# Performance work log

Measured on AMD Instinct MI355X. Metric: run time of the kernel, lower is better.

The kernel has to match this reference:

```python
import jax, jax.numpy as jnp
import numpy as np
import math

B, C, H, W = 16, 512, 32, 32
GROUPS = 32
EPS = 1e-5


def group_norm(x, w, b):
    # x: [B, C, H, W]; normalize within each of GROUPS channel groups over (C//G, H, W)
    Bx, Cx, Hx, Wx = x.shape
    xg = x.reshape(Bx, GROUPS, Cx // GROUPS, Hx, Wx)
    mean = xg.mean(axis=(2, 3, 4), keepdims=True)
    var = xg.var(axis=(2, 3, 4), keepdims=True)
    xg = (xg - mean) * jax.lax.rsqrt(var + EPS)
    xn = xg.reshape(Bx, Cx, Hx, Wx)
    return xn * w[None, :, None, None] + b[None, :, None, None]


def setup_inputs() -> dict:
    key = jax.random.key(0)
    ks = jax.random.split(key, 4)
    x = jax.random.normal(ks[0], (B, C, H, W), dtype=jnp.float32)
    gn_w = jnp.ones((C,), dtype=jnp.float32)
    gn_b = jnp.zeros((C,), dtype=jnp.float32)
    # Conv2d 1x1 weights as [out, in] matrices; PyTorch default init scale
    qkv_w = jax.random.normal(ks[1], (3 * C, C), dtype=jnp.float32) * (1.0 / math.sqrt(C))
    qkv_b = jnp.zeros((3 * C,), dtype=jnp.float32)
    out_w = jax.random.normal(ks[2], (C, C), dtype=jnp.float32) * (1.0 / math.sqrt(C))
    out_b = jnp.zeros((C,), dtype=jnp.float32)
    return {"x": x, "gn_w": gn_w, "gn_b": gn_b, "qkv_w": qkv_w,
            "qkv_b": qkv_b, "out_w": out_w, "out_b": out_b}


def reference(x, gn_w, gn_b, qkv_w, qkv_b, out_w, out_b):
    Bx, Cx, Hx, Wx = x.shape
    N = Hx * Wx
    h = group_norm(x, gn_w, gn_b)                       # [B, C, H, W]
    hf = h.reshape(Bx, Cx, N)                           # [B, C, N]
    # 1x1 conv == channel matmul
    qkv = jnp.einsum('oc,bcn->bon', qkv_w, hf) + qkv_b[None, :, None]  # [B, 3C, N]
    q, k, v = jnp.split(qkv, 3, axis=1)                 # each [B, C, N]
    q = q.transpose(0, 2, 1)                            # [B, N, C]
    v = v.transpose(0, 2, 1)                            # [B, N, C]
    scale = 1.0 / math.sqrt(Cx)
    attn = jnp.einsum('bnc,bcm->bnm', q, k) * scale     # [B, N, N]
    attn = jax.nn.softmax(attn, axis=-1)
    o = jnp.einsum('bnm,bmc->bnc', attn, v)             # [B, N, C]
    o = o.transpose(0, 2, 1)                            # [B, C, N]
    o = jnp.einsum('oc,bcn->bon', out_w, o) + out_b[None, :, None]
    return x + o.reshape(Bx, Cx, Hx, Wx)
```

## Files before the change

### kernel.cpp

```cpp
#include <hip/hip_runtime.h>

typedef unsigned short u16;
typedef short short8 __attribute__((ext_vector_type(8)));
typedef float floatx4 __attribute__((ext_vector_type(4)));
typedef u16 u16x4 __attribute__((ext_vector_type(4)));
typedef u16 u16x8 __attribute__((ext_vector_type(8)));

#define DEVI __device__ __forceinline__

DEVI u16 f2bf(float x) {
    union { float f; unsigned u; } c; c.f = x;
    unsigned u = c.u;
    u += 0x7fffu + ((u >> 16) & 1u);
    return (u16)(u >> 16);
}
DEVI float bf2f(u16 h) {
    union { unsigned u; float f; } c; c.u = ((unsigned)h) << 16;
    return c.f;
}

DEVI void gload_lds16(const void* g, void* l) {
    auto gp = (const __attribute__((address_space(1))) unsigned*)(unsigned long long)g;
    auto lp = (__attribute__((address_space(3))) unsigned*)(unsigned)(unsigned long long)l;
    __builtin_amdgcn_global_load_lds(gp, lp, 16, 0, 0);
}

__global__ __launch_bounds__(256) void gn_fused_kernel(const float* __restrict__ x,
                                                       const float* __restrict__ w,
                                                       const float* __restrict__ bb,
                                                       u16* __restrict__ h) {
    const int bg = blockIdx.x;
    const int b = bg >> 5, g = bg & 31;
    const float* xg = x + (long long)bg * 16384;
    const int n0 = threadIdx.x * 4;

    float4 xv[16];
    float s = 0.f, s2 = 0.f;
    #pragma unroll
    for (int cc = 0; cc < 16; cc++) {
        xv[cc] = *(const float4*)&xg[cc * 1024 + n0];
        s  += xv[cc].x + xv[cc].y + xv[cc].z + xv[cc].w;
        s2 += xv[cc].x*xv[cc].x + xv[cc].y*xv[cc].y + xv[cc].z*xv[cc].z + xv[cc].w*xv[cc].w;
    }
    #pragma unroll
    for (int m = 1; m < 64; m <<= 1) { s += __shfl_xor(s, m, 64); s2 += __shfl_xor(s2, m, 64); }
    __shared__ float rs[4], rq[4];
    if ((threadIdx.x & 63) == 0) { rs[threadIdx.x >> 6] = s; rq[threadIdx.x >> 6] = s2; }
    __syncthreads();
    float mean = (rs[0] + rs[1] + rs[2] + rs[3]) * (1.f / 16384.f);
    float var  = (rq[0] + rq[1] + rq[2] + rq[3]) * (1.f / 16384.f) - mean * mean;
    float rstd = rsqrtf(var + 1e-5f);

    u16x8 o[4][2];
    #pragma unroll
    for (int cc = 0; cc < 16; cc++) {
        int c = g * 16 + cc;
        float sc = w[c] * rstd;
        float sh = bb[c] - mean * sc;
        o[0][cc >> 3][cc & 7] = f2bf(xv[cc].x * sc + sh);
        o[1][cc >> 3][cc & 7] = f2bf(xv[cc].y * sc + sh);
        o[2][cc >> 3][cc & 7] = f2bf(xv[cc].z * sc + sh);
        o[3][cc >> 3][cc & 7] = f2bf(xv[cc].w * sc + sh);
    }
    u16* hb = h + ((long long)b * 1024 + n0) * 512 + g * 16;
    #pragma unroll
    for (int k = 0; k < 4; k++) {
        *(u16x8*)&hb[(long long)k * 512]     = o[k][0];
        *(u16x8*)&hb[(long long)k * 512 + 8] = o[k][1];
    }
}

__global__ __launch_bounds__(256) void wconv_kernel(const float* __restrict__ w1, u16* __restrict__ o1,
                                                    const float* __restrict__ w2, u16* __restrict__ o2) {
    int i = blockIdx.x * 256 + threadIdx.x;
    const float* src; u16* dst; int j;
    if (i < 196608) { src = w1; dst = o1; j = i; }
    else            { src = w2; dst = o2; j = i - 196608; }
    float4 v = *(const float4*)&src[j * 4];
    u16x4 p; p[0] = f2bf(v.x); p[1] = f2bf(v.y); p[2] = f2bf(v.z); p[3] = f2bf(v.w);
    *(u16x4*)&dst[j * 4] = p;
}

__global__ __launch_bounds__(256) void softmax_kernel(u16* __restrict__ P) {
    const int lid  = blockIdx.x;
    const int xcd  = lid & 7;
    const int slot = lid >> 3;
    const int j    = slot >> 8;
    const int w    = slot & 255;
    const int z    = xcd + 8 * j;
    const int wave = threadIdx.x >> 6, lane = threadIdx.x & 63;
    const long long row = (long long)z * 1024 + w * 4 + wave;
    u16* p = P + row * 1024 + lane * 16;
    u16x8 a = *(u16x8*)p;
    u16x8 b = *(u16x8*)(p + 8);
    float v[16];
    #pragma unroll
    for (int k = 0; k < 8; k++) { v[k] = bf2f(a[k]); v[8+k] = bf2f(b[k]); }
    float mx = v[0];
    #pragma unroll
    for (int k = 1; k < 16; k++) mx = fmaxf(mx, v[k]);
    #pragma unroll
    for (int m = 1; m < 64; m <<= 1) mx = fmaxf(mx, __shfl_xor(mx, m, 64));
    float s = 0.f;
    #pragma unroll
    for (int k = 0; k < 16; k++) { v[k] = __expf(v[k] - mx); s += v[k]; }
    #pragma unroll
    for (int m = 1; m < 64; m <<= 1) s += __shfl_xor(s, m, 64);
    float inv = 1.f / s;
    #pragma unroll
    for (int k = 0; k < 8; k++) { a[k] = f2bf(v[k]*inv); b[k] = f2bf(v[8+k]*inv); }
    *(u16x8*)p = a;
    *(u16x8*)(p + 8) = b;
}

template <int MODE, int NX, int NY>
__global__ __launch_bounds__(256, 3)
void gemm_bt_kernel(const u16* __restrict__ A, const u16* __restrict__ Bt,
                    void* __restrict__ C0,
                    const float* __restrict__ bias, const float* __restrict__ res,
                    float scale, int lda, int ldb, int ldc,
                    long long sA, long long sB, long long sC, long long sR, int K) {
    int bx, by, bz;
    if (NX > 0) {
        const int lid  = blockIdx.x;
        const int xcd  = lid & 7;
        const int slot = lid >> 3;
        const int per  = NX * NY;
        const int j    = slot / per;
        const int w    = slot - j * per;
        bz = xcd + 8 * j;
        bx = w % NX;
        by = w / NX;
    } else {
        bx = blockIdx.x; by = blockIdx.y; bz = blockIdx.z;
    }
    const int t    = threadIdx.x;
    const int lane = t & 63;
    const int wave = t >> 6;
    const int m0   = by * 128;
    const int n0   = bx * 128;
    A  += (long long)bz * sA;
    Bt += (long long)bz * sB;

    __shared__ __align__(16) u16 smem[16384];
    u16* As = smem;
    u16* Bs = smem + 8192;

    const int wm = wave >> 1, wn = wave & 1;
    const int quad = lane >> 4, lrow = lane & 15;

    floatx4 acc[4][4];
    #pragma unroll
    for (int i = 0; i < 4; i++)
        #pragma unroll
        for (int j = 0; j < 4; j++)
            #pragma unroll
            for (int r = 0; r < 4; r++) acc[i][j][r] = 0.f;

    const int rowA = t >> 2;
    const int kch  = (t & 3) * 8;
    const u16* Ag = A  + (long long)(m0 + rowA) * lda + kch;
    const u16* Bg = Bt + (long long)(n0 + rowA) * ldb + kch;
    u16* Al = &As[t * 8];
    u16* Bl = &Bs[t * 8];
    const long long a64 = (long long)64 * lda;
    const long long b64 = (long long)64 * ldb;

    for (int k0 = 0; k0 < K; k0 += 64) {
        gload_lds16(Ag + k0,            Al);
        gload_lds16(Ag + k0 + a64,      Al + 2048);
        gload_lds16(Ag + k0 + 32,       Al + 4096);
        gload_lds16(Ag + k0 + 32 + a64, Al + 6144);
        gload_lds16(Bg + k0,            Bl);
        gload_lds16(Bg + k0 + b64,      Bl + 2048);
        gload_lds16(Bg + k0 + 32,       Bl + 4096);
        gload_lds16(Bg + k0 + 32 + b64, Bl + 6144);
        __syncthreads();
        #pragma unroll
        for (int kk = 0; kk < 2; kk++) {
            short8 af[4], bfr[4];
            #pragma unroll
            for (int i = 0; i < 4; i++)
                af[i] = *(const short8*)&As[kk*4096 + (wm*64 + i*16 + lrow)*32 + quad*8];
            #pragma unroll
            for (int j = 0; j < 4; j++)
                bfr[j] = *(const short8*)&Bs[kk*4096 + (wn*64 + j*16 + lrow)*32 + quad*8];
            #pragma unroll
            for (int i = 0; i < 4; i++)
                #pragma unroll
                for (int j = 0; j < 4; j++)
                    acc[i][j] = __builtin_amdgcn_mfma_f32_16x16x32_bf16(af[i], bfr[j], acc[i][j], 0, 0, 0);
        }
        __syncthreads();
    }

    const int ST = 136;

    if (MODE == 1) {
        #pragma unroll
        for (int p = 0; p < 4; p++) {
            if (p) __syncthreads();
            if (wm == (p >> 1)) {
                #pragma unroll
                for (int ii = 0; ii < 2; ii++) {
                    const int i = (p & 1) * 2 + ii;
                    const int row = ii * 16 + quad * 4;
                    #pragma unroll
                    for (int j = 0; j < 4; j++) {
                        const int cB = wn * 64 + j * 16 + lrow;
                        #pragma unroll
                        for (int r = 0; r < 4; r++)
                            smem[(row + r) * ST + cB] = f2bf(acc[i][j][r] * scale);
                    }
                }
            }
            __syncthreads();
            const int rr = t >> 3, cc = (t & 7) * 16;
            u16x8 a0 = *(u16x8*)&smem[rr * ST + cc];
            u16x8 a1 = *(u16x8*)&smem[rr * ST + cc + 8];
            u16* Cp = (u16*)C0 + (long long)bz * sC + (long long)(m0 + p * 32 + rr) * ldc + n0 + cc;
            *(u16x8*)Cp = a0;
            *(u16x8*)(Cp + 8) = a1;
        }
    } else if (MODE == 2) {
        #pragma unroll
        for (int p = 0; p < 4; p++) {
            if (p) __syncthreads();
            if (wn == (p >> 1)) {
                #pragma unroll
                for (int jj = 0; jj < 2; jj++) {
                    const int j = (p & 1) * 2 + jj;
                    const int row = jj * 16 + lrow;
                    #pragma unroll
                    for (int i = 0; i < 4; i++) {
                        const int mmL = wm * 64 + i * 16 + quad * 4;
                        u16x4 pk;
                        #pragma unroll
                        for (int r = 0; r < 4; r++)
                            pk[r] = f2bf(acc[i][j][r] + bias[m0 + mmL + r]);
                        *(u16x4*)&smem[row * ST + mmL] = pk;
                    }
                }
            }
            __syncthreads();
            const int rr = t >> 3, cc = (t & 7) * 16;
            u16x8 a0 = *(u16x8*)&smem[rr * ST + cc];
            u16x8 a1 = *(u16x8*)&smem[rr * ST + cc + 8];
            u16* Cp = (u16*)C0 + (long long)(n0 + p * 32 + rr) * ldc + m0 + cc;
            *(u16x8*)Cp = a0;
            *(u16x8*)(Cp + 8) = a1;
        }
    } else {
        float* smf = (float*)smem;
        const int SF = 132;
        float* C = (float*)C0 + (long long)bz * sC;
        const float* rz = res + (long long)bz * sR;
        #pragma unroll
        for (int p = 0; p < 8; p++) {
            if (p) __syncthreads();
            if (wm == (p >> 2)) {
                const int i = p & 3;
                #pragma unroll
                for (int j = 0; j < 4; j++) {
                    const int cB = wn * 64 + j * 16 + lrow;
                    #pragma unroll
                    for (int r = 0; r < 4; r++)
                        smf[(quad * 4 + r) * SF + cB] =
                            acc[i][j][r] + bias[m0 + p * 16 + quad * 4 + r];
                }
            }
            __syncthreads();
            const int rr = t >> 4, cc = (t & 15) * 8;
            const long long gro = (long long)(m0 + p * 16 + rr) * ldc + n0 + cc;
            float4 rv0 = *(const float4*)&rz[gro];
            float4 rv1 = *(const float4*)&rz[gro + 4];
            float4 ov0, ov1;
            ov0.x = smf[rr*SF + cc + 0] + rv0.x;
            ov0.y = smf[rr*SF + cc + 1] + rv0.y;
            ov0.z = smf[rr*SF + cc + 2] + rv0.z;
            ov0.w = smf[rr*SF + cc + 3] + rv0.w;
            ov1.x = smf[rr*SF + cc + 4] + rv1.x;
            ov1.y = smf[rr*SF + cc + 5] + rv1.y;
            ov1.z = smf[rr*SF + cc + 6] + rv1.z;
            ov1.w = smf[rr*SF + cc + 7] + rv1.w;
            *(float4*)&C[gro]     = ov0;
            *(float4*)&C[gro + 4] = ov1;
        }
    }
}

extern "C" void kernel_launch(void* const* d_in, const int* in_sizes, int n_in,
                              void* d_out, int out_size, void* d_ws, size_t ws_size,
                              hipStream_t stream) {
    (void)in_sizes; (void)n_in; (void)out_size; (void)ws_size;
    const float* x     = (const float*)d_in[0];
    const float* gn_w  = (const float*)d_in[1];
    const float* gn_b  = (const float*)d_in[2];
    const float* qkv_w = (const float*)d_in[3];
    const float* qkv_b = (const float*)d_in[4];
    const float* out_w = (const float*)d_in[5];
    const float* out_b = (const float*)d_in[6];
    float* out = (float*)d_out;

    char* ws = (char*)d_ws;
    u16*  h_t   = (u16*)ws;  ws += (size_t)16*1024*512*2;
    u16*  qkv_t = (u16*)ws;  ws += (size_t)16*1024*1536*2;
    u16*  vprm  = (u16*)ws;  ws += (size_t)512*16384*2;
    u16*  S     = (u16*)ws;  ws += (size_t)16*1024*1024*2;
    u16*  wq    = (u16*)ws;  ws += (size_t)1536*512*2;
    u16*  wo    = (u16*)ws;  ws += (size_t)512*512*2;

    wconv_kernel<<<1024, 256, 0, stream>>>(qkv_w, wq, out_w, wo);
    gn_fused_kernel<<<512, 256, 0, stream>>>(x, gn_w, gn_b, h_t);

    gemm_bt_kernel<2, 0, 0><<<dim3(128, 12, 1), 256, 0, stream>>>(
        wq, h_t, qkv_t, qkv_b, nullptr, 1.0f,
        512, 512, 1536, 0, 0, 0, 0, 512);

    gemm_bt_kernel<1, 0, 0><<<dim3(128, 4, 1), 256, 0, stream>>>(
        wo, qkv_t + 1024, vprm, nullptr, nullptr, 1.0f,
        512, 1536, 16384, 0, 0, 0, 0, 512);

    gemm_bt_kernel<1, 8, 8><<<1024, 256, 0, stream>>>(
        qkv_t, qkv_t + 512, S, nullptr, nullptr, 0.044194173824159216f,
        1536, 1536, 1024,
        (long long)1024*1536, (long long)1024*1536, (long long)1024*1024, 0, 512);

    softmax_kernel<<<4096, 256, 0, stream>>>(S);

    gemm_bt_kernel<0, 8, 4><<<512, 256, 0, stream>>>(
        vprm, S, out, out_b, x, 1.0f,
        16384, 1024, 1024,
        1024, (long long)1024*1024, (long long)512*1024, (long long)512*1024, 1024);
}
```

Measured before the change: 217.6 us.

## Fold V projection into output projection weights to drop V GEMM

Precomputes Wo·Wv as a combined 512x512 weight matrix and Wo·bv+bo as a combined bias. The V-then-output-projection GEMM (K=512 over qkv columns) becomes a single GEMM on h, and the QKV GEMM now produces only Q and K (1024 columns). This removes one third of the QKV projection FLOPs and the V write/read traffic. In exchange it adds a small weight-transpose, a weight GEMM and a bias kernel, plus an extra bf16 rounding of the fused weights, which may change numerics slightly.

```diff
diff --git a/kernel.cpp b/kernel.cpp
--- a/kernel.cpp
+++ b/kernel.cpp
@@ -70,15 +70,53 @@
     }
 }
 
-__global__ __launch_bounds__(256) void wconv_kernel(const float* __restrict__ w1, u16* __restrict__ o1,
-                                                    const float* __restrict__ w2, u16* __restrict__ o2) {
-    int i = blockIdx.x * 256 + threadIdx.x;
-    const float* src; u16* dst; int j;
-    if (i < 196608) { src = w1; dst = o1; j = i; }
-    else            { src = w2; dst = o2; j = i - 196608; }
-    float4 v = *(const float4*)&src[j * 4];
-    u16x4 p; p[0] = f2bf(v.x); p[1] = f2bf(v.y); p[2] = f2bf(v.z); p[3] = f2bf(v.w);
-    *(u16x4*)&dst[j * 4] = p;
+__global__ __launch_bounds__(256) void wprep_kernel(const float* __restrict__ qkv_w,
+                                                    u16* __restrict__ wqk,
+                                                    const float* __restrict__ out_w,
+                                                    u16* __restrict__ wo,
+                                                    u16* __restrict__ wvT) {
+    const int blk = blockIdx.x;
+    if (blk < 768) {
+        int i = blk * 256 + threadIdx.x;
+        const float* src; u16* dst; int j;
+        if (i < 131072) { src = qkv_w; dst = wqk; j = i; }
+        else            { src = out_w; dst = wo;  j = i - 131072; }
+        float4 v = *(const float4*)&src[j * 4];
+        u16x4 p; p[0] = f2bf(v.x); p[1] = f2bf(v.y); p[2] = f2bf(v.z); p[3] = f2bf(v.w);
+        *(u16x4*)&dst[j * 4] = p;
+    } else {
+        const int tt = blk - 768;
+        const int tr = tt >> 4, tc = tt & 15;
+        const int tx = threadIdx.x & 31, ty = threadIdx.x >> 5;
+        __shared__ float tl[32][33];
+        #pragma unroll
+        for (int p = 0; p < 4; p++) {
+            int cvl = ty + p * 8;
+            tl[cvl][tx] = qkv_w[(long long)(1024 + tc * 32 + cvl) * 512 + tr * 32 + tx];
+        }
+        __syncthreads();
+        #pragma unroll
+        for (int p = 0; p < 4; p++) {
+            int cil = ty + p * 8;
+            wvT[(long long)(tr * 32 + cil) * 512 + tc * 32 + tx] = f2bf(tl[tx][cil]);
+        }
+    }
+}
+
+__global__ __launch_bounds__(256) void bvo_kernel(const float* __restrict__ out_w,
+                                                  const float* __restrict__ qkv_b,
+                                                  const float* __restrict__ out_b,
+                                                  float* __restrict__ biasout) {
+    const int c = blockIdx.x * 256 + threadIdx.x;
+    const float4* wr = (const float4*)(out_w + (long long)c * 512);
+    const float4* bv = (const float4*)(qkv_b + 1024);
+    float s = 0.f;
+    #pragma unroll 4
+    for (int i = 0; i < 128; i++) {
+        float4 a = wr[i], b = bv[i];
+        s += a.x*b.x + a.y*b.y + a.z*b.z + a.w*b.w;
+    }
+    biasout[c] = out_b[c] + s;
 }
 
 __global__ __launch_bounds__(256) void softmax_kernel(u16* __restrict__ P) {
@@ -304,32 +342,40 @@
 
     char* ws = (char*)d_ws;
     u16*  h_t   = (u16*)ws;  ws += (size_t)16*1024*512*2;
-    u16*  qkv_t = (u16*)ws;  ws += (size_t)16*1024*1536*2;
+    u16*  qkv_t = (u16*)ws;  ws += (size_t)16*1024*1024*2;
     u16*  vprm  = (u16*)ws;  ws += (size_t)512*16384*2;
     u16*  S     = (u16*)ws;  ws += (size_t)16*1024*1024*2;
-    u16*  wq    = (u16*)ws;  ws += (size_t)1536*512*2;
+    u16*  wqk   = (u16*)ws;  ws += (size_t)1024*512*2;
     u16*  wo    = (u16*)ws;  ws += (size_t)512*512*2;
-
-    wconv_kernel<<<1024, 256, 0, stream>>>(qkv_w, wq, out_w, wo);
+    u16*  wvT   = (u16*)ws;  ws += (size_t)512*512*2;
+    u16*  wvo   = (u16*)ws;  ws += (size_t)512*512*2;
+    float* biasout = (float*)ws; ws += (size_t)512*4;
+
+    wprep_kernel<<<1024, 256, 0, stream>>>(qkv_w, wqk, out_w, wo, wvT);
+    bvo_kernel<<<2, 256, 0, stream>>>(out_w, qkv_b, out_b, biasout);
     gn_fused_kernel<<<512, 256, 0, stream>>>(x, gn_w, gn_b, h_t);
 
-    gemm_bt_kernel<2, 0, 0><<<dim3(128, 12, 1), 256, 0, stream>>>(
-        wq, h_t, qkv_t, qkv_b, nullptr, 1.0f,
-        512, 512, 1536, 0, 0, 0, 0, 512);
+    gemm_bt_kernel<1, 0, 0><<<dim3(4, 4, 1), 256, 0, stream>>>(
+        wo, wvT, wvo, nullptr, nullptr, 1.0f,
+        512, 512, 512, 0, 0, 0, 0, 512);
+
+    gemm_bt_kernel<2, 0, 0><<<dim3(128, 8, 1), 256, 0, stream>>>(
+        wqk, h_t, qkv_t, qkv_b, nullptr, 1.0f,
+        512, 512, 1024, 0, 0, 0, 0, 512);
 
     gemm_bt_kernel<1, 0, 0><<<dim3(128, 4, 1), 256, 0, stream>>>(
-        wo, qkv_t + 1024, vprm, nullptr, nullptr, 1.0f,
-        512, 1536, 16384, 0, 0, 0, 0, 512);
+        wvo, h_t, vprm, nullptr, nullptr, 1.0f,
+        512, 512, 16384, 0, 0, 0, 0, 512);
 
     gemm_bt_kernel<1, 8, 8><<<1024, 256, 0, stream>>>(
         qkv_t, qkv_t + 512, S, nullptr, nullptr, 0.044194173824159216f,
-        1536, 1536, 1024,
-        (long long)1024*1536, (long long)1024*1536, (long long)1024*1024, 0, 512);
+        1024, 1024, 1024,
+        (long long)1024*1024, (long long)1024*1024, (long long)1024*1024, 0, 512);
 
     softmax_kernel<<<4096, 256, 0, stream>>>(S);
 
     gemm_bt_kernel<0, 8, 4><<<512, 256, 0, stream>>>(
-        vprm, S, out, out_b, x, 1.0f,
+        vprm, S, out, biasout, x, 1.0f,
         16384, 1024, 1024,
         1024, (long long)1024*1024, (long long)512*1024, (long long)512*1024, 1024);
 }
```

Result: slower. 231.3 us (+6.3%).

## Fuse softmax into QK^T epilogue and the PV GEMM load path

Applied to the files above, without the earlier changes.

Drops the standalone softmax kernel. The QK^T GEMM epilogue now writes per-tile partial row sums of exp(logit). A small reduce kernel turns these into inverse row sums. The final GEMM exponentiates the stored bf16 logits while loading them into LDS and applies the 1/l normalization, bias and residual in its epilogue. This removes a full read/write pass over the score matrix. The costs are redundant exp work per output tile and synchronous register-staged loads in place of async global-to-LDS copies. It also skips the max subtraction, so large logits could overflow.

```diff
diff --git a/kernel.cpp b/kernel.cpp
--- a/kernel.cpp
+++ b/kernel.cpp
@@ -13,6 +13,10 @@
     unsigned u = c.u;
     u += 0x7fffu + ((u >> 16) & 1u);
     return (u16)(u >> 16);
+}
+DEVI u16 f2bf_fast(float x) {
+    union { float f; unsigned u; } c; c.f = x;
+    return (u16)((c.u + 0x8000u) >> 16);
 }
 DEVI float bf2f(u16 h) {
     union { unsigned u; float f; } c; c.u = ((unsigned)h) << 16;
@@ -81,43 +85,22 @@
     *(u16x4*)&dst[j * 4] = p;
 }
 
-__global__ __launch_bounds__(256) void softmax_kernel(u16* __restrict__ P) {
-    const int lid  = blockIdx.x;
-    const int xcd  = lid & 7;
-    const int slot = lid >> 3;
-    const int j    = slot >> 8;
-    const int w    = slot & 255;
-    const int z    = xcd + 8 * j;
-    const int wave = threadIdx.x >> 6, lane = threadIdx.x & 63;
-    const long long row = (long long)z * 1024 + w * 4 + wave;
-    u16* p = P + row * 1024 + lane * 16;
-    u16x8 a = *(u16x8*)p;
-    u16x8 b = *(u16x8*)(p + 8);
-    float v[16];
-    #pragma unroll
-    for (int k = 0; k < 8; k++) { v[k] = bf2f(a[k]); v[8+k] = bf2f(b[k]); }
-    float mx = v[0];
-    #pragma unroll
-    for (int k = 1; k < 16; k++) mx = fmaxf(mx, v[k]);
-    #pragma unroll
-    for (int m = 1; m < 64; m <<= 1) mx = fmaxf(mx, __shfl_xor(mx, m, 64));
-    float s = 0.f;
-    #pragma unroll
-    for (int k = 0; k < 16; k++) { v[k] = __expf(v[k] - mx); s += v[k]; }
-    #pragma unroll
-    for (int m = 1; m < 64; m <<= 1) s += __shfl_xor(s, m, 64);
-    float inv = 1.f / s;
-    #pragma unroll
-    for (int k = 0; k < 8; k++) { a[k] = f2bf(v[k]*inv); b[k] = f2bf(v[8+k]*inv); }
-    *(u16x8*)p = a;
-    *(u16x8*)(p + 8) = b;
-}
-
-template <int MODE, int NX, int NY>
+__global__ __launch_bounds__(256) void lreduce_kernel(const float* __restrict__ ps,
+                                                      float* __restrict__ invl) {
+    int i = blockIdx.x * 256 + threadIdx.x;
+    int z = i >> 10, n = i & 1023;
+    float l = 0.f;
+    #pragma unroll
+    for (int kb = 0; kb < 8; kb++) l += ps[((z * 8 + kb) << 10) + n];
+    invl[i] = 1.f / l;
+}
+
+template <int MODE, int NX, int NY, bool STATS>
 __global__ __launch_bounds__(256, 3)
 void gemm_bt_kernel(const u16* __restrict__ A, const u16* __restrict__ Bt,
                     void* __restrict__ C0,
                     const float* __restrict__ bias, const float* __restrict__ res,
+                    float* __restrict__ aux,
                     float scale, int lda, int ldb, int ldc,
                     long long sA, long long sB, long long sC, long long sR, int K) {
     int bx, by, bz;
@@ -165,16 +148,31 @@
     u16* Bl = &Bs[t * 8];
     const long long a64 = (long long)64 * lda;
     const long long b64 = (long long)64 * ldb;
+    const u16* Bg3 = Bt + (long long)n0 * ldb;
 
     for (int k0 = 0; k0 < K; k0 += 64) {
         gload_lds16(Ag + k0,            Al);
         gload_lds16(Ag + k0 + a64,      Al + 2048);
         gload_lds16(Ag + k0 + 32,       Al + 4096);
         gload_lds16(Ag + k0 + 32 + a64, Al + 6144);
-        gload_lds16(Bg + k0,            Bl);
-        gload_lds16(Bg + k0 + b64,      Bl + 2048);
-        gload_lds16(Bg + k0 + 32,       Bl + 4096);
-        gload_lds16(Bg + k0 + 32 + b64, Bl + 6144);
+        if (MODE != 3) {
+            gload_lds16(Bg + k0,            Bl);
+            gload_lds16(Bg + k0 + b64,      Bl + 2048);
+            gload_lds16(Bg + k0 + 32,       Bl + 4096);
+            gload_lds16(Bg + k0 + 32 + b64, Bl + 6144);
+        } else {
+            #pragma unroll
+            for (int q = 0; q < 4; q++) {
+                const int row = ((q & 1) ? 64 : 0) + (t >> 2);
+                const int kc  = (q >> 1) * 32 + (t & 3) * 8;
+                u16x8 sv = *(const u16x8*)&Bg3[(long long)row * ldb + k0 + kc];
+                u16x8 ev;
+                #pragma unroll
+                for (int e = 0; e < 8; e++)
+                    ev[e] = f2bf_fast(__expf(bf2f(sv[e])));
+                *(u16x8*)&Bs[q * 2048 + t * 8] = ev;
+            }
+        }
         __syncthreads();
         #pragma unroll
         for (int kk = 0; kk < 2; kk++) {
@@ -221,6 +219,16 @@
             u16* Cp = (u16*)C0 + (long long)bz * sC + (long long)(m0 + p * 32 + rr) * ldc + n0 + cc;
             *(u16x8*)Cp = a0;
             *(u16x8*)(Cp + 8) = a1;
+            if (STATS) {
+                float ls = 0.f;
+                #pragma unroll
+                for (int e = 0; e < 8; e++)
+                    ls += __expf(bf2f(a0[e])) + __expf(bf2f(a1[e]));
+                #pragma unroll
+                for (int m2 = 1; m2 < 8; m2 <<= 1) ls += __shfl_xor(ls, m2, 8);
+                if ((t & 7) == 0)
+                    aux[((long long)(bz * 8 + bx)) * 1024 + m0 + p * 32 + rr] = ls;
+            }
         }
     } else if (MODE == 2) {
         #pragma unroll
@@ -255,6 +263,7 @@
         const int SF = 132;
         float* C = (float*)C0 + (long long)bz * sC;
         const float* rz = res + (long long)bz * sR;
+        const float* il = aux + (long long)bz * 1024;
         #pragma unroll
         for (int p = 0; p < 8; p++) {
             if (p) __syncthreads();
@@ -265,24 +274,26 @@
                     const int cB = wn * 64 + j * 16 + lrow;
                     #pragma unroll
                     for (int r = 0; r < 4; r++)
-                        smf[(quad * 4 + r) * SF + cB] =
-                            acc[i][j][r] + bias[m0 + p * 16 + quad * 4 + r];
+                        smf[(quad * 4 + r) * SF + cB] = acc[i][j][r];
                 }
             }
             __syncthreads();
             const int rr = t >> 4, cc = (t & 15) * 8;
+            const float bsv = bias[m0 + p * 16 + rr];
+            float4 il0 = *(const float4*)&il[n0 + cc];
+            float4 il1 = *(const float4*)&il[n0 + cc + 4];
             const long long gro = (long long)(m0 + p * 16 + rr) * ldc + n0 + cc;
             float4 rv0 = *(const float4*)&rz[gro];
             float4 rv1 = *(const float4*)&rz[gro + 4];
             float4 ov0, ov1;
-            ov0.x = smf[rr*SF + cc + 0] + rv0.x;
-            ov0.y = smf[rr*SF + cc + 1] + rv0.y;
-            ov0.z = smf[rr*SF + cc + 2] + rv0.z;
-            ov0.w = smf[rr*SF + cc + 3] + rv0.w;
-            ov1.x = smf[rr*SF + cc + 4] + rv1.x;
-            ov1.y = smf[rr*SF + cc + 5] + rv1.y;
-            ov1.z = smf[rr*SF + cc + 6] + rv1.z;
-            ov1.w = smf[rr*SF + cc + 7] + rv1.w;
+            ov0.x = smf[rr*SF + cc + 0] * il0.x + bsv + rv0.x;
+            ov0.y = smf[rr*SF + cc + 1] * il0.y + bsv + rv0.y;
+            ov0.z = smf[rr*SF + cc + 2] * il0.z + bsv + rv0.z;
+            ov0.w = smf[rr*SF + cc + 3] * il0.w + bsv + rv0.w;
+            ov1.x = smf[rr*SF + cc + 4] * il1.x + bsv + rv1.x;
+            ov1.y = smf[rr*SF + cc + 5] * il1.y + bsv + rv1.y;
+            ov1.z = smf[rr*SF + cc + 6] * il1.z + bsv + rv1.z;
+            ov1.w = smf[rr*SF + cc + 7] * il1.w + bsv + rv1.w;
             *(float4*)&C[gro]     = ov0;
             *(float4*)&C[gro + 4] = ov1;
         }
@@ -309,27 +320,29 @@
     u16*  S     = (u16*)ws;  ws += (size_t)16*1024*1024*2;
     u16*  wq    = (u16*)ws;  ws += (size_t)1536*512*2;
     u16*  wo    = (u16*)ws;  ws += (size_t)512*512*2;
+    float* psum = (float*)ws; ws += (size_t)16*8*1024*4;
+    float* invl = (float*)ws; ws += (size_t)16*1024*4;
 
     wconv_kernel<<<1024, 256, 0, stream>>>(qkv_w, wq, out_w, wo);
     gn_fused_kernel<<<512, 256, 0, stream>>>(x, gn_w, gn_b, h_t);
 
-    gemm_bt_kernel<2, 0, 0><<<dim3(128, 12, 1), 256, 0, stream>>>(
-        wq, h_t, qkv_t, qkv_b, nullptr, 1.0f,
+    gemm_bt_kernel<2, 0, 0, false><<<dim3(128, 12, 1), 256, 0, stream>>>(
+        wq, h_t, qkv_t, qkv_b, nullptr, nullptr, 1.0f,
         512, 512, 1536, 0, 0, 0, 0, 512);
 
-    gemm_bt_kernel<1, 0, 0><<<dim3(128, 4, 1), 256, 0, stream>>>(
-        wo, qkv_t + 1024, vprm, nullptr, nullptr, 1.0f,
+    gemm_bt_kernel<1, 0, 0, false><<<dim3(128, 4, 1), 256, 0, stream>>>(
+        wo, qkv_t + 1024, vprm, nullptr, nullptr, nullptr, 1.0f,
         512, 1536, 16384, 0, 0, 0, 0, 512);
 
-    gemm_bt_kernel<1, 8, 8><<<1024, 256, 0, stream>>>(
-        qkv_t, qkv_t + 512, S, nullptr, nullptr, 0.044194173824159216f,
+    gemm_bt_kernel<1, 8, 8, true><<<1024, 256, 0, stream>>>(
+        qkv_t, qkv_t + 512, S, nullptr, nullptr, psum, 0.044194173824159216f,
         1536, 1536, 1024,
         (long long)1024*1536, (long long)1024*1536, (long long)1024*1024, 0, 512);
 
-    softmax_kernel<<<4096, 256, 0, stream>>>(S);
-
-    gemm_bt_kernel<0, 8, 4><<<512, 256, 0, stream>>>(
-        vprm, S, out, out_b, x, 1.0f,
+    lreduce_kernel<<<64, 256, 0, stream>>>(psum, invl);
+
+    gemm_bt_kernel<3, 8, 4, false><<<512, 256, 0, stream>>>(
+        vprm, S, out, out_b, x, invl, 1.0f,
         16384, 1024, 1024,
         1024, (long long)1024*1024, (long long)512*1024, (long long)512*1024, 1024);
 }
```

After: 213.6 us. About the same (-1.9%).
